# Performance work log

Hardware: AMD Instinct MI355X
Metric: run time of the kernel (lower is better)

Reference implementation:

```python
import jax, jax.numpy as jnp
import numpy as np

GROUP_NORM_EPS = 1e-6
NUM_GROUPS = 32


def group_norm(x, gamma, beta, num_groups=NUM_GROUPS, eps=GROUP_NORM_EPS):
    B, H, W, C = x.shape
    g = num_groups
    xg = x.reshape(B, H, W, g, C // g)
    mean = jnp.mean(xg, axis=(1, 2, 4), keepdims=True)
    var = jnp.var(xg, axis=(1, 2, 4), keepdims=True)
    xn = ((xg - mean) * jax.lax.rsqrt(var + eps)).reshape(B, H, W, C)
    return xn * gamma + beta


def setup_inputs() -> dict:
    key = jax.random.key(0)
    ks = jax.random.split(key, 6)
    B, H, W, C = 4, 64, 64, 512
    scale = 1.0 / np.sqrt(C)
    return {
        "x": jax.random.normal(ks[0], (B, H, W, C), jnp.float32),
        "gn_gamma": jnp.ones((C,), jnp.float32),
        "gn_beta": jnp.zeros((C,), jnp.float32),
        "wq": jax.random.normal(ks[1], (C, C), jnp.float32) * scale,
        "bq": jnp.zeros((C,), jnp.float32),
        "wk": jax.random.normal(ks[2], (C, C), jnp.float32) * scale,
        "bk": jnp.zeros((C,), jnp.float32),
        "wv": jax.random.normal(ks[3], (C, C), jnp.float32) * scale,
        "bv": jnp.zeros((C,), jnp.float32),
        "wo": jax.random.normal(ks[4], (C, C), jnp.float32) * scale,
        "bo": jnp.zeros((C,), jnp.float32),
    }


def reference(x, gn_gamma, gn_beta, wq, bq, wk, bk, wv, bv, wo, bo):
    B, H, W, C = x.shape
    h = group_norm(x, gn_gamma, gn_beta)
    q = h @ wq + bq  # [B,H,W,C]
    k = h @ wk + bk
    v = h @ wv + bv
    N = H * W
    qf = q.reshape(B, N, C)
    kf = k.reshape(B, N, C)
    vf = v.reshape(B, N, C)
    # full spatial self-attention: [B, N, N] score matrix
    scores = jnp.einsum('bnc,bmc->bnm', qf, kf) * (C ** -0.5)
    attn = jax.nn.softmax(scores, axis=-1)
    out = jnp.einsum('bnm,bmc->bnc', attn, vf).reshape(B, H, W, C)
    out = out @ wo + bo
    return out + x
```

## Files before the change

### kernel.cpp

```cpp
#include <hip/hip_runtime.h>

typedef __bf16 bf16x8 __attribute__((ext_vector_type(8)));
typedef float  f32x4  __attribute__((ext_vector_type(4)));
typedef float  f32x16 __attribute__((ext_vector_type(16)));
typedef unsigned long long u64x2 __attribute__((ext_vector_type(2)));
typedef unsigned short u16;
typedef unsigned short us4 __attribute__((ext_vector_type(4)));

__device__ __forceinline__ u16 f2bf(float f) {
  __bf16 h = (__bf16)f;
  return __builtin_bit_cast(u16, h);
}

__device__ __forceinline__ void gload16(const void* g, void* l) {
  __builtin_amdgcn_global_load_lds(
      (const __attribute__((address_space(1))) unsigned int*)(g),
      (__attribute__((address_space(3))) unsigned int*)(l), 16, 0, 0);
}

__device__ __forceinline__ void barrier_lgkm() {
  asm volatile("s_waitcnt lgkmcnt(0)" ::: "memory");
  __builtin_amdgcn_s_barrier();
  asm volatile("" ::: "memory");
}
template <int N> __device__ __forceinline__ void vmwait() {
  asm volatile("s_waitcnt vmcnt(%0)" :: "n"(N) : "memory");
}

__global__ void gn_partial(const float* __restrict__ x, float* __restrict__ part) {
  const int chunk = blockIdx.x, g = blockIdx.y, b = blockIdx.z;
  const int tid = threadIdx.x;
  float s = 0.f, ss = 0.f;
  const float* xb = x + ((size_t)(b * 4096 + chunk * 512)) * 512 + g * 16;
  for (int i = tid; i < 2048; i += 256) {
    const int sp = i >> 2, c4 = (i & 3) << 2;
    const float4 v = *(const float4*)(xb + (size_t)sp * 512 + c4);
    s  += v.x + v.y + v.z + v.w;
    ss += v.x * v.x + v.y * v.y + v.z * v.z + v.w * v.w;
  }
  for (int m = 32; m; m >>= 1) { s += __shfl_xor(s, m); ss += __shfl_xor(ss, m); }
  __shared__ float red[8];
  const int w = tid >> 6;
  if ((tid & 63) == 0) { red[w * 2] = s; red[w * 2 + 1] = ss; }
  __syncthreads();
  if (tid == 0) {
    float S = 0.f, SS = 0.f;
    for (int i = 0; i < 4; ++i) { S += red[2 * i]; SS += red[2 * i + 1]; }
    const int idx = ((b * 32 + g) * 8 + chunk) * 2;
    part[idx] = S; part[idx + 1] = SS;
  }
}

__global__ void gn_finalize(const float* __restrict__ part, float* __restrict__ stats) {
  const int t = threadIdx.x;
  if (t < 128) {
    float S = 0.f, SS = 0.f;
    for (int i = 0; i < 8; ++i) { S += part[(t * 8 + i) * 2]; SS += part[(t * 8 + i) * 2 + 1]; }
    const float mean = S * (1.0f / 65536.0f);
    const float var  = SS * (1.0f / 65536.0f) - mean * mean;
    stats[t * 2] = mean;
    stats[t * 2 + 1] = rsqrtf(var + 1e-6f);
  }
}

__global__ void gn_apply(const float* __restrict__ x, const float* __restrict__ gamma,
                         const float* __restrict__ beta, const float* __restrict__ stats,
                         u16* __restrict__ h) {
  const size_t i = (size_t)blockIdx.x * 256 + threadIdx.x;
  const size_t e = i * 4;
  const int c = (int)(e & 511);
  const int b = (int)(e >> 21);
  const int g = c >> 4;
  const float mean = stats[(b * 32 + g) * 2];
  const float rstd = stats[(b * 32 + g) * 2 + 1];
  const float4 xv = *(const float4*)(x + e);
  const float4 gv = *(const float4*)(gamma + c);
  const float4 bv = *(const float4*)(beta + c);
  us4 hv;
  hv.x = f2bf((xv.x - mean) * rstd * gv.x + bv.x);
  hv.y = f2bf((xv.y - mean) * rstd * gv.y + bv.y);
  hv.z = f2bf((xv.z - mean) * rstd * gv.z + bv.z);
  hv.w = f2bf((xv.w - mean) * rstd * gv.w + bv.w);
  *(us4*)(h + e) = hv;
}

__global__ void wcast_t4(const float* __restrict__ wq, const float* __restrict__ wk,
                         const float* __restrict__ wv, const float* __restrict__ wo,
                         u16* __restrict__ wT) {
  const int idx = blockIdx.x * 256 + threadIdx.x;
  const int which = idx >> 18;
  const int rr = idx & 262143;
  const float* w = (which == 0) ? wq : (which == 1) ? wk : (which == 2) ? wv : wo;
  const int n = rr >> 9, k = rr & 511;
  wT[idx] = f2bf(w[k * 512 + n]);
}

#define GEMM_STAGE(buf, t)                                                       \
  {                                                                              \
    const int k0 = (t) * 32;                                                     \
    _Pragma("unroll")                                                            \
    for (int i = 0; i < 2; ++i) {                                                \
      const int cid = tid + i * 256;                                             \
      const int row = cid >> 2, cb = cid & 3;                                    \
      const int sc = (cb ^ (row & 3)) << 3;                                      \
      gload16(A + (size_t)(brow + row) * 512 + k0 + sc, &lA[buf][cid << 3]);     \
      gload16(Bt + (size_t)(bcol0 + row) * 512 + k0 + sc, &lB[buf][cid << 3]);   \
    }                                                                            \
  }

#define GEMM_MAIN                                                                \
  const f32x4 zero4 = {0.f, 0.f, 0.f, 0.f};                                      \
  f32x4 acc[4][4];                                                               \
  _Pragma("unroll") for (int a_ = 0; a_ < 4; ++a_)                               \
  _Pragma("unroll") for (int b_ = 0; b_ < 4; ++b_) acc[a_][b_] = zero4;          \
  GEMM_STAGE(0, 0);                                                              \
  asm volatile("s_waitcnt vmcnt(0)" ::: "memory");                               \
  __syncthreads();                                                               \
  int buf = 0;                                                                   \
  for (int t = 0; t < 16; ++t) {                                                 \
    if (t < 15) GEMM_STAGE(buf ^ 1, t + 1);                                      \
    bf16x8 af[4], bfv[4];                                                        \
    _Pragma("unroll") for (int f = 0; f < 4; ++f) {                              \
      const int ra = wr * 64 + f * 16 + l15;                                     \
      af[f] = *(const bf16x8*)(&lA[buf][(ra << 5) + ((lq ^ (ra & 3)) << 3)]);    \
      const int rb = wc * 64 + f * 16 + l15;                                     \
      bfv[f] = *(const bf16x8*)(&lB[buf][(rb << 5) + ((lq ^ (rb & 3)) << 3)]);   \
    }                                                                            \
    _Pragma("unroll") for (int fa = 0; fa < 4; ++fa)                             \
    _Pragma("unroll") for (int fb = 0; fb < 4; ++fb)                             \
      acc[fa][fb] = __builtin_amdgcn_mfma_f32_16x16x32_bf16(af[fa], bfv[fb],     \
                                                            acc[fa][fb], 0, 0, 0);\
    asm volatile("s_waitcnt vmcnt(0)" ::: "memory");                             \
    __syncthreads();                                                             \
    buf ^= 1;                                                                    \
  }

__global__ __launch_bounds__(256)
void gemm_oproj(const u16* __restrict__ A, const u16* __restrict__ Bt,
                const float* __restrict__ bias, const float* __restrict__ resid,
                float* __restrict__ Cout) {
  const int tid = threadIdx.x;
  const int wid = tid >> 6, l = tid & 63;
  const int wr = wid >> 1, wc = wid & 1;
  const int l15 = l & 15, lq = l >> 4;
  const int brow = blockIdx.x * 128, bcol0 = blockIdx.y * 128;
  __shared__ u16 lA[2][4096];
  __shared__ u16 lB[2][4096];
  GEMM_MAIN
#pragma unroll
  for (int fa = 0; fa < 4; ++fa)
#pragma unroll
    for (int fb = 0; fb < 4; ++fb) {
      const int col = bcol0 + wc * 64 + fb * 16 + l15;
      const float bv = bias[col];
#pragma unroll
      for (int i = 0; i < 4; ++i) {
        const int row = brow + wr * 64 + fa * 16 + lq * 4 + i;
        const size_t idx = (size_t)row * 512 + col;
        Cout[idx] = acc[fa][fb][i] + bv + resid[idx];
      }
    }
}

__global__ __launch_bounds__(256)
void gemm_qkv(const u16* __restrict__ A, const u16* __restrict__ wT,
              const float* __restrict__ bq, const float* __restrict__ bk,
              const float* __restrict__ bv_, u16* __restrict__ q,
              u16* __restrict__ k, u16* __restrict__ v8, float qs) {
  const int tid = threadIdx.x;
  const int wid = tid >> 6, l = tid & 63;
  const int wr = wid >> 1, wc = wid & 1;
  const int l15 = l & 15, lq = l >> 4;
  const int which = blockIdx.y >> 2;
  const int brow = blockIdx.x * 128, bcol0 = (blockIdx.y & 3) * 128;
  const u16* Bt = wT + which * 262144;
  const float* bias = (which == 0) ? bq : ((which == 1) ? bk : bv_);
  __shared__ u16 lA[2][4096];
  __shared__ u16 lB[2][4096];
  GEMM_MAIN
#pragma unroll
  for (int fa = 0; fa < 4; ++fa)
#pragma unroll
    for (int fb = 0; fb < 4; ++fb) {
      const int col = bcol0 + wc * 64 + fb * 16 + l15;
      const float bb_ = bias[col];
#pragma unroll
      for (int i = 0; i < 4; ++i) {
        const int row = brow + wr * 64 + fa * 16 + lq * 4 + i;
        const float v = acc[fa][fb][i] + bb_;
        if (which == 0) {
          q[(size_t)row * 512 + col] = f2bf(v * qs);
        } else if (which == 1) {
          k[(size_t)row * 512 + col] = f2bf(v);
        } else {
          const int bb = row >> 12, n = row & 4095;
          v8[((size_t)(bb * 512 + (n >> 3))) * 4096 +
             (size_t)((col ^ ((n >> 3) & 3)) << 3) + (n & 7)] = f2bf(v);
        }
      }
    }
}

__global__ __launch_bounds__(512, 2)
void attn_kernel(const u16* __restrict__ Q, const u16* __restrict__ K,
                 const u16* __restrict__ V8, u16* __restrict__ Oo) {
  const int bid = blockIdx.x;
  const int b = bid & 3, qb = bid >> 2;
  const int tid = threadIdx.x;
  const int wid = tid >> 6, l = tid & 63;
  const int l31 = l & 31, lh = l >> 5;

  __shared__ __align__(16) char lds[141072];
  const int PB = 131072, AB = 140288, FL = 140800, LR = 140816;

  const u16* Kb = K + (size_t)b * 2097152;
  const u16* Vb = V8 + (size_t)b * 2097152;

  const f32x16 z16 = {0.f,0.f,0.f,0.f, 0.f,0.f,0.f,0.f, 0.f,0.f,0.f,0.f, 0.f,0.f,0.f,0.f};

  if (wid >= 6) {
    const int stid = (wid - 6) * 64 + l;
    {
      char* kd = lds;
#pragma unroll
      for (int i = 0; i < 16; ++i) {
        const int cid = stid + i * 128;
        const int ob = cid << 4;
        const int n_ = ob >> 10;
        const int cb = (ob & 1023) ^ ((n_ & 15) << 4);
        gload16(Kb + (size_t)n_ * 512 + (cb >> 1), kd + ob);
      }
    }
    vmwait<0>();
    barrier_lgkm();
    for (int t = 0; t < 128; ++t) {
      if (t < 127) {
        const u16* ks = Kb + (size_t)(t + 1) * 16384;
        char* kd = lds + (((t + 1) & 1) << 15);
#pragma unroll
        for (int i = 0; i < 16; ++i) {
          const int cid = stid + i * 128;
          const int ob = cid << 4;
          const int n_ = ob >> 10;
          const int cb = (ob & 1023) ^ ((n_ & 15) << 4);
          gload16(ks + (size_t)n_ * 512 + (cb >> 1), kd + ob);
        }
      }
      {
        const u16* vs = Vb + (size_t)t * 16384;
        char* vd = lds + 65536 + ((t & 1) << 15);
#pragma unroll
        for (int i = 0; i < 16; ++i) {
          const int cid = stid + i * 128;
          gload16(vs + (size_t)cid * 8, vd + (cid << 4));
        }
      }
      vmwait<0>();
      barrier_lgkm();
    }
    barrier_lgkm();
  } else if (wid < 2) {
    const int qh = wid;
    barrier_lgkm();
    bf16x8 qf[32];
    {
      const u16* qp = Q + ((size_t)(b * 4096 + qb * 64 + qh * 32 + l31)) * 512 + lh * 8;
#pragma unroll
      for (int kk = 0; kk < 32; ++kk) qf[kk] = *(const bf16x8*)(qp + kk * 16);
    }
    float m_ = -3e38f, l_ = 0.f;
    const int kxor = (l31 & 15) << 4;
    for (int t = 0; t < 128; ++t) {
      const char* kb = lds + ((t & 1) << 15) + l31 * 1024;
      f32x16 a0 = z16, a1 = z16;
#pragma unroll
      for (int kk = 0; kk < 32; kk += 2) {
        const bf16x8 k0 = *(const bf16x8*)(kb + ((kk * 32 + lh * 16) ^ kxor));
        a0 = __builtin_amdgcn_mfma_f32_32x32x16_bf16(k0, qf[kk], a0, 0, 0, 0);
        const bf16x8 k1 = *(const bf16x8*)(kb + (((kk + 1) * 32 + lh * 16) ^ kxor));
        a1 = __builtin_amdgcn_mfma_f32_32x32x16_bf16(k1, qf[kk + 1], a1, 0, 0, 0);
      }
      const f32x16 s = a0 + a1;
      float tmax = fmaxf(s[0], s[1]);
#pragma unroll
      for (int r2 = 2; r2 < 16; ++r2) tmax = fmaxf(tmax, s[r2]);
      tmax = fmaxf(tmax, __shfl_xor(tmax, 32));
      const bool need = tmax > m_ + 8.0f;
      const float mn = need ? tmax : m_;
      const float al = need ? __expf(m_ - mn) : 1.0f;
      float p[16];
#pragma unroll
      for (int r2 = 0; r2 < 16; ++r2) p[r2] = __expf(s[r2] - mn);
      float ps = 0.f;
#pragma unroll
      for (int r2 = 0; r2 < 16; ++r2) ps += p[r2];
      ps += __shfl_xor(ps, 32);
      l_ = l_ * al + ps;
      m_ = mn;
      char* prow = lds + PB + (t & 1) * 4608 + (qh * 32 + l31) * 72;
#pragma unroll
      for (int rg = 0; rg < 4; ++rg) {
        us4 pk4;
        pk4.x = f2bf(p[rg * 4 + 0]); pk4.y = f2bf(p[rg * 4 + 1]);
        pk4.z = f2bf(p[rg * 4 + 2]); pk4.w = f2bf(p[rg * 4 + 3]);
        *(unsigned long long*)(prow + rg * 16 + lh * 8) =
            __builtin_bit_cast(unsigned long long, pk4);
      }
      if (lh == 0) *(float*)(lds + AB + (t & 1) * 256 + (qh * 32 + l31) * 4) = al;
      const bool anyn = __any(need);
      if (l == 0) *(int*)(lds + FL + ((t & 1) * 2 + qh) * 4) = anyn ? 1 : 0;
      barrier_lgkm();
    }
    if (lh == 0) *(float*)(lds + LR + (qh * 32 + l31) * 4) = l_;
    barrier_lgkm();
  } else {
    const int dq = wid - 2;
    barrier_lgkm();
    f32x16 o[2][4];
#pragma unroll
    for (int qt = 0; qt < 2; ++qt)
#pragma unroll
      for (int f = 0; f < 4; ++f) o[qt][f] = z16;

    auto pv_apply = [&](int pb_) {
      bf16x8 pa[2][2];
#pragma unroll
      for (int qt = 0; qt < 2; ++qt)
#pragma unroll
        for (int h2 = 0; h2 < 2; ++h2) {
          const char* pr = lds + PB + pb_ * 4608 + (qt * 32 + l31) * 72 + h2 * 32 + lh * 16;
          u64x2 w2;
          w2[0] = *(const unsigned long long*)pr;
          w2[1] = *(const unsigned long long*)(pr + 8);
          pa[qt][h2] = __builtin_bit_cast(bf16x8, w2);
        }
      const int fl = *(const int*)(lds + FL + pb_ * 8) |
                     *(const int*)(lds + FL + pb_ * 8 + 4);
      if (fl) {
#pragma unroll
        for (int qt = 0; qt < 2; ++qt)
#pragma unroll
          for (int rg = 0; rg < 16; ++rg) {
            const int cr = (rg & 3) + 8 * (rg >> 2) + 4 * lh;
            const float av = *(const float*)(lds + AB + pb_ * 256 + (qt * 32 + cr) * 4);
#pragma unroll
            for (int f = 0; f < 4; ++f) o[qt][f][rg] *= av;
          }
      }
      const char* vb = lds + 65536 + (pb_ << 15);
#pragma unroll
      for (int f = 0; f < 4; ++f) {
        const int d = dq * 128 + f * 32 + l31;
#pragma unroll
        for (int h2 = 0; h2 < 2; ++h2) {
          const int c4 = h2 * 2 + lh;
          const bf16x8 vf = *(const bf16x8*)(vb + (size_t)(c4 * 512 + (d ^ c4)) * 16);
          o[0][f] = __builtin_amdgcn_mfma_f32_32x32x16_bf16(pa[0][h2], vf, o[0][f], 0, 0, 0);
          o[1][f] = __builtin_amdgcn_mfma_f32_32x32x16_bf16(pa[1][h2], vf, o[1][f], 0, 0, 0);
        }
      }
    };

    for (int t = 0; t < 128; ++t) {
      if (t > 0) pv_apply((t - 1) & 1);
      barrier_lgkm();
    }
    pv_apply(1);
    barrier_lgkm();
#pragma unroll
    for (int qt = 0; qt < 2; ++qt)
#pragma unroll
      for (int rg = 0; rg < 16; ++rg) {
        const int cr = (rg & 3) + 8 * (rg >> 2) + 4 * lh;
        const float li = 1.0f / *(const float*)(lds + LR + (qt * 32 + cr) * 4);
        u16* orow = Oo + ((size_t)(b * 4096 + qb * 64 + qt * 32 + cr)) * 512 + dq * 128 + l31;
#pragma unroll
        for (int f = 0; f < 4; ++f) orow[f * 32] = f2bf(o[qt][f][rg] * li);
      }
  }
}

extern "C" void kernel_launch(void* const* d_in, const int* in_sizes, int n_in,
                              void* d_out, int out_size, void* d_ws, size_t ws_size,
                              hipStream_t stream) {
  const float* x     = (const float*)d_in[0];
  const float* gamma = (const float*)d_in[1];
  const float* beta  = (const float*)d_in[2];
  const float* wq    = (const float*)d_in[3];
  const float* bq    = (const float*)d_in[4];
  const float* wk    = (const float*)d_in[5];
  const float* bk    = (const float*)d_in[6];
  const float* wv    = (const float*)d_in[7];
  const float* bv    = (const float*)d_in[8];
  const float* wo    = (const float*)d_in[9];
  const float* bo    = (const float*)d_in[10];
  float* out = (float*)d_out;

  char* ws = (char*)d_ws;
  const size_t SZ = (size_t)16384 * 512;
  u16* h    = (u16*)(ws);
  u16* q    = (u16*)(ws + SZ * 2);
  u16* k    = (u16*)(ws + SZ * 4);
  u16* v8   = (u16*)(ws + SZ * 6);
  u16* aout = (u16*)(ws + SZ * 8);
  u16* wT   = (u16*)(ws + SZ * 10);
  float* part  = (float*)(ws + SZ * 10 + 4 * 262144 * 2);
  float* stats = part + 2048;

  gn_partial<<<dim3(8, 32, 4), 256, 0, stream>>>(x, part);
  gn_finalize<<<1, 128, 0, stream>>>(part, stats);
  gn_apply<<<8192, 256, 0, stream>>>(x, gamma, beta, stats, h);

  wcast_t4<<<4096, 256, 0, stream>>>(wq, wk, wv, wo, wT);

  const float qs = 0.044194173824159216f;
  gemm_qkv<<<dim3(128, 12), 256, 0, stream>>>(h, wT, bq, bk, bv, q, k, v8, qs);

  attn_kernel<<<256, 512, 0, stream>>>(q, k, v8, aout);

  gemm_oproj<<<dim3(128, 4), 256, 0, stream>>>(aout, wT + 3 * 262144, bo, x, out);
}
```

Baseline: 259.4 us.

## Drop dedicated loader waves; PV waves stream K via LDS and V into registers

Removes the two loader wavefronts from the attention kernel. The four PV waves now issue the next K tile's async global-to-LDS copies and load V directly from global memory into double-buffered registers, which removes the V region from LDS and nearly halves LDS use. The QK wave's inner loop gets four independent MFMA accumulators instead of two to expose more parallelism. The risks are V global-load latency landing on the PV critical path, higher register pressure in the PV waves, and a per-step vmcnt wait whose ordering could be fragile.

```diff
diff --git a/kernel.cpp b/kernel.cpp
--- a/kernel.cpp
+++ b/kernel.cpp
@@ -201,7 +201,7 @@
     }
 }
 
-__global__ __launch_bounds__(512, 2)
+__global__ __launch_bounds__(384)
 void attn_kernel(const u16* __restrict__ Q, const u16* __restrict__ K,
                  const u16* __restrict__ V8, u16* __restrict__ Oo) {
   const int bid = blockIdx.x;
@@ -210,77 +210,40 @@
   const int wid = tid >> 6, l = tid & 63;
   const int l31 = l & 31, lh = l >> 5;
 
-  __shared__ __align__(16) char lds[141072];
-  const int PB = 131072, AB = 140288, FL = 140800, LR = 140816;
+  __shared__ __align__(16) char lds[75536];
+  const int PB = 65536, AB = 74752, FL = 75264, LR = 75280;
 
   const u16* Kb = K + (size_t)b * 2097152;
   const u16* Vb = V8 + (size_t)b * 2097152;
 
   const f32x16 z16 = {0.f,0.f,0.f,0.f, 0.f,0.f,0.f,0.f, 0.f,0.f,0.f,0.f, 0.f,0.f,0.f,0.f};
 
-  if (wid >= 6) {
-    const int stid = (wid - 6) * 64 + l;
-    {
-      char* kd = lds;
-#pragma unroll
-      for (int i = 0; i < 16; ++i) {
-        const int cid = stid + i * 128;
-        const int ob = cid << 4;
-        const int n_ = ob >> 10;
-        const int cb = (ob & 1023) ^ ((n_ & 15) << 4);
-        gload16(Kb + (size_t)n_ * 512 + (cb >> 1), kd + ob);
-      }
-    }
-    vmwait<0>();
-    barrier_lgkm();
-    for (int t = 0; t < 128; ++t) {
-      if (t < 127) {
-        const u16* ks = Kb + (size_t)(t + 1) * 16384;
-        char* kd = lds + (((t + 1) & 1) << 15);
-#pragma unroll
-        for (int i = 0; i < 16; ++i) {
-          const int cid = stid + i * 128;
-          const int ob = cid << 4;
-          const int n_ = ob >> 10;
-          const int cb = (ob & 1023) ^ ((n_ & 15) << 4);
-          gload16(ks + (size_t)n_ * 512 + (cb >> 1), kd + ob);
-        }
-      }
-      {
-        const u16* vs = Vb + (size_t)t * 16384;
-        char* vd = lds + 65536 + ((t & 1) << 15);
-#pragma unroll
-        for (int i = 0; i < 16; ++i) {
-          const int cid = stid + i * 128;
-          gload16(vs + (size_t)cid * 8, vd + (cid << 4));
-        }
-      }
-      vmwait<0>();
-      barrier_lgkm();
-    }
-    barrier_lgkm();
-  } else if (wid < 2) {
+  if (wid < 2) {
     const int qh = wid;
-    barrier_lgkm();
     bf16x8 qf[32];
     {
       const u16* qp = Q + ((size_t)(b * 4096 + qb * 64 + qh * 32 + l31)) * 512 + lh * 8;
 #pragma unroll
       for (int kk = 0; kk < 32; ++kk) qf[kk] = *(const bf16x8*)(qp + kk * 16);
     }
+    barrier_lgkm();
     float m_ = -3e38f, l_ = 0.f;
     const int kxor = (l31 & 15) << 4;
     for (int t = 0; t < 128; ++t) {
       const char* kb = lds + ((t & 1) << 15) + l31 * 1024;
-      f32x16 a0 = z16, a1 = z16;
-#pragma unroll
-      for (int kk = 0; kk < 32; kk += 2) {
+      f32x16 a0 = z16, a1 = z16, a2 = z16, a3 = z16;
+#pragma unroll
+      for (int kk = 0; kk < 32; kk += 4) {
         const bf16x8 k0 = *(const bf16x8*)(kb + ((kk * 32 + lh * 16) ^ kxor));
         a0 = __builtin_amdgcn_mfma_f32_32x32x16_bf16(k0, qf[kk], a0, 0, 0, 0);
         const bf16x8 k1 = *(const bf16x8*)(kb + (((kk + 1) * 32 + lh * 16) ^ kxor));
         a1 = __builtin_amdgcn_mfma_f32_32x32x16_bf16(k1, qf[kk + 1], a1, 0, 0, 0);
-      }
-      const f32x16 s = a0 + a1;
+        const bf16x8 k2 = *(const bf16x8*)(kb + (((kk + 2) * 32 + lh * 16) ^ kxor));
+        a2 = __builtin_amdgcn_mfma_f32_32x32x16_bf16(k2, qf[kk + 2], a2, 0, 0, 0);
+        const bf16x8 k3 = *(const bf16x8*)(kb + (((kk + 3) * 32 + lh * 16) ^ kxor));
+        a3 = __builtin_amdgcn_mfma_f32_32x32x16_bf16(k3, qf[kk + 3], a3, 0, 0, 0);
+      }
+      const f32x16 s = (a0 + a1) + (a2 + a3);
       float tmax = fmaxf(s[0], s[1]);
 #pragma unroll
       for (int r2 = 2; r2 < 16; ++r2) tmax = fmaxf(tmax, s[r2]);
@@ -315,58 +278,98 @@
     barrier_lgkm();
   } else {
     const int dq = wid - 2;
+    const int stid = (wid - 2) * 64 + l;
+    {
+      char* kd = lds;
+#pragma unroll
+      for (int i = 0; i < 8; ++i) {
+        const int cid = stid + i * 256;
+        const int ob = cid << 4;
+        const int n_ = ob >> 10;
+        const int cb = (ob & 1023) ^ ((n_ & 15) << 4);
+        gload16(Kb + (size_t)n_ * 512 + (cb >> 1), kd + ob);
+      }
+    }
+    vmwait<0>();
     barrier_lgkm();
     f32x16 o[2][4];
 #pragma unroll
     for (int qt = 0; qt < 2; ++qt)
 #pragma unroll
       for (int f = 0; f < 4; ++f) o[qt][f] = z16;
-
-    auto pv_apply = [&](int pb_) {
-      bf16x8 pa[2][2];
-#pragma unroll
-      for (int qt = 0; qt < 2; ++qt)
-#pragma unroll
-        for (int h2 = 0; h2 < 2; ++h2) {
-          const char* pr = lds + PB + pb_ * 4608 + (qt * 32 + l31) * 72 + h2 * 32 + lh * 16;
-          u64x2 w2;
-          w2[0] = *(const unsigned long long*)pr;
-          w2[1] = *(const unsigned long long*)(pr + 8);
-          pa[qt][h2] = __builtin_bit_cast(bf16x8, w2);
-        }
-      const int fl = *(const int*)(lds + FL + pb_ * 8) |
-                     *(const int*)(lds + FL + pb_ * 8 + 4);
-      if (fl) {
-#pragma unroll
-        for (int qt = 0; qt < 2; ++qt)
-#pragma unroll
-          for (int rg = 0; rg < 16; ++rg) {
-            const int cr = (rg & 3) + 8 * (rg >> 2) + 4 * lh;
-            const float av = *(const float*)(lds + AB + pb_ * 256 + (qt * 32 + cr) * 4);
-#pragma unroll
-            for (int f = 0; f < 4; ++f) o[qt][f][rg] *= av;
-          }
-      }
-      const char* vb = lds + 65536 + (pb_ << 15);
-#pragma unroll
-      for (int f = 0; f < 4; ++f) {
-        const int d = dq * 128 + f * 32 + l31;
-#pragma unroll
-        for (int h2 = 0; h2 < 2; ++h2) {
-          const int c4 = h2 * 2 + lh;
-          const bf16x8 vf = *(const bf16x8*)(vb + (size_t)(c4 * 512 + (d ^ c4)) * 16);
-          o[0][f] = __builtin_amdgcn_mfma_f32_32x32x16_bf16(pa[0][h2], vf, o[0][f], 0, 0, 0);
-          o[1][f] = __builtin_amdgcn_mfma_f32_32x32x16_bf16(pa[1][h2], vf, o[1][f], 0, 0, 0);
-        }
-      }
-    };
-
-    for (int t = 0; t < 128; ++t) {
-      if (t > 0) pv_apply((t - 1) & 1);
-      barrier_lgkm();
-    }
-    pv_apply(1);
+    bf16x8 vrA[8], vrB[8];
+
+#define PV_APPLY(PB_, VUSE)                                                      \
+    {                                                                            \
+      bf16x8 pa[2][2];                                                           \
+      _Pragma("unroll") for (int qt = 0; qt < 2; ++qt)                           \
+      _Pragma("unroll") for (int h2 = 0; h2 < 2; ++h2) {                         \
+        const char* pr = lds + PB + (PB_) * 4608 + (qt * 32 + l31) * 72 +        \
+                         h2 * 32 + lh * 16;                                      \
+        u64x2 w2;                                                                \
+        w2[0] = *(const unsigned long long*)pr;                                  \
+        w2[1] = *(const unsigned long long*)(pr + 8);                            \
+        pa[qt][h2] = __builtin_bit_cast(bf16x8, w2);                             \
+      }                                                                          \
+      const int fl = *(const int*)(lds + FL + (PB_) * 8) |                       \
+                     *(const int*)(lds + FL + (PB_) * 8 + 4);                    \
+      if (fl) {                                                                  \
+        _Pragma("unroll") for (int qt = 0; qt < 2; ++qt)                         \
+        _Pragma("unroll") for (int rg = 0; rg < 16; ++rg) {                      \
+          const int cr = (rg & 3) + 8 * (rg >> 2) + 4 * lh;                      \
+          const float av = *(const float*)(lds + AB + (PB_) * 256 +              \
+                                           (qt * 32 + cr) * 4);                  \
+          _Pragma("unroll") for (int f = 0; f < 4; ++f) o[qt][f][rg] *= av;      \
+        }                                                                        \
+      }                                                                          \
+      _Pragma("unroll") for (int f = 0; f < 4; ++f)                              \
+      _Pragma("unroll") for (int h2 = 0; h2 < 2; ++h2) {                         \
+        o[0][f] = __builtin_amdgcn_mfma_f32_32x32x16_bf16(pa[0][h2],             \
+                      VUSE[f * 2 + h2], o[0][f], 0, 0, 0);                       \
+        o[1][f] = __builtin_amdgcn_mfma_f32_32x32x16_bf16(pa[1][h2],             \
+                      VUSE[f * 2 + h2], o[1][f], 0, 0, 0);                       \
+      }                                                                          \
+    }
+
+#define PV_STEP(T, VUSE, VLOAD)                                                  \
+    {                                                                            \
+      const int t_ = (T);                                                        \
+      if (t_ < 127) {                                                            \
+        const u16* ks = Kb + (size_t)(t_ + 1) * 16384;                           \
+        char* kd = lds + (((t_ + 1) & 1) << 15);                                 \
+        _Pragma("unroll") for (int i = 0; i < 8; ++i) {                          \
+          const int cid = stid + i * 256;                                        \
+          const int ob = cid << 4;                                               \
+          const int n_ = ob >> 10;                                               \
+          const int cb = (ob & 1023) ^ ((n_ & 15) << 4);                         \
+          gload16(ks + (size_t)n_ * 512 + (cb >> 1), kd + ob);                   \
+        }                                                                        \
+      }                                                                          \
+      vmwait<8>();                                       \
+      if (t_ > 0) { PV_APPLY((t_ - 1) & 1, VUSE) }                               \
+      {                                                                          \
+        const u16* vsrc = Vb + (size_t)t_ * 16384;                               \
+        _Pragma("unroll") for (int f = 0; f < 4; ++f)                            \
+        _Pragma("unroll") for (int h2 = 0; h2 < 2; ++h2) {                       \
+          const int c4 = h2 * 2 + lh;                                            \
+          const int d = dq * 128 + f * 32 + l31;                                 \
+          VLOAD[f * 2 + h2] =                                                    \
+              *(const bf16x8*)(vsrc + ((size_t)(c4 * 512 + (d ^ c4)) << 3));     \
+        }                                                                        \
+      }                                                                          \
+      vmwait<8>();                              \
+      barrier_lgkm();                                                            \
+    }
+
+    for (int tt = 0; tt < 64; ++tt) {
+      PV_STEP(2 * tt,     vrB, vrA)
+      PV_STEP(2 * tt + 1, vrA, vrB)
+    }
+    vmwait<0>();
+    PV_APPLY(1, vrB)
     barrier_lgkm();
+#undef PV_STEP
+#undef PV_APPLY
 #pragma unroll
     for (int qt = 0; qt < 2; ++qt)
 #pragma unroll
@@ -416,7 +419,7 @@
   const float qs = 0.044194173824159216f;
   gemm_qkv<<<dim3(128, 12), 256, 0, stream>>>(h, wT, bq, bk, bv, q, k, v8, qs);
 
-  attn_kernel<<<256, 512, 0, stream>>>(q, k, v8, aout);
+  attn_kernel<<<256, 384, 0, stream>>>(q, k, v8, aout);
 
   gemm_oproj<<<dim3(128, 4), 256, 0, stream>>>(aout, wT + 3 * 262144, bo, x, out);
 }
```

Result: slower. 265.6 us (+2.4%).
